# Kernel tuning notes

Measured on AMD Instinct MI355X. Metric: run time of the kernel, lower is better.

Reference implementation:

```python
import jax, jax.numpy as jnp
import numpy as np

HEADS = 8
DIM_HEAD = 64
C = 512              # in_channels == inner_dim = heads*dim_head
WIN = 7              # window size implied by rel_pos table (2*7-1 = 13)
EPS = 1e-5


def setup_inputs() -> dict:
    key = jax.random.key(0)
    ks = jax.random.split(key, 6)
    B = 2048
    inner = HEADS * DIM_HEAD
    x = jax.random.normal(ks[0], (B, C, WIN, WIN), dtype=jnp.float32)
    gamma = jnp.ones((C,), dtype=jnp.float32)
    beta = jnp.zeros((C,), dtype=jnp.float32)
    w_qkv = jax.random.normal(ks[1], (C, 3 * inner), dtype=jnp.float32) / np.sqrt(C)
    rel_table = jax.random.normal(ks[2], (2 * WIN - 1, 2 * WIN - 1, HEADS), dtype=jnp.float32)
    w_out = jax.random.normal(ks[3], (inner, C), dtype=jnp.float32) / np.sqrt(inner)
    b_out = jnp.zeros((C,), dtype=jnp.float32)
    return {"x": x, "gamma": gamma, "beta": beta, "w_qkv": w_qkv,
            "rel_table": rel_table, "w_out": w_out, "b_out": b_out}


def _rel_pos_bias(rel_table, H, W):
    # Swin-style additive bias: bias[h, i, j] = table[hi-hj+H-1, wi-wj+W-1, h]
    hh = jnp.arange(H)
    ww = jnp.arange(W)
    hi = jnp.repeat(hh, W)          # [N] row index of each flattened position
    wi = jnp.tile(ww, H)            # [N] col index
    dh = hi[:, None] - hi[None, :] + (H - 1)   # [N, N]
    dw = wi[:, None] - wi[None, :] + (W - 1)   # [N, N]
    bias = rel_table[dh, dw]        # [N, N, heads]
    return jnp.transpose(bias, (2, 0, 1))      # [heads, N, N]


def reference(x, gamma, beta, w_qkv, rel_table, w_out, b_out):
    B, Cc, H, W = x.shape
    N = H * W
    shortcut = x
    xs = jnp.transpose(x.reshape(B, Cc, N), (0, 2, 1))   # [B, N, C]
    # LayerNorm over channel dim
    mu = jnp.mean(xs, axis=-1, keepdims=True)
    var = jnp.var(xs, axis=-1, keepdims=True)
    xn = (xs - mu) * jax.lax.rsqrt(var + EPS) * gamma + beta
    qkv = xn @ w_qkv                                      # [B, N, 3*inner]
    q, k, v = jnp.split(qkv, 3, axis=-1)
    def heads(t):
        return jnp.transpose(t.reshape(B, N, HEADS, DIM_HEAD), (0, 2, 1, 3))  # [B,h,N,d]
    q, k, v = heads(q), heads(k), heads(v)
    scale = DIM_HEAD ** -0.5
    dots = jnp.einsum('bhnd,bhmd->bhnm', q, k) * scale   # [B,h,N,N]
    dots = dots + _rel_pos_bias(rel_table, H, W)[None]   # add Swin-style bias
    attn = jax.nn.softmax(dots, axis=-1)
    out = jnp.einsum('bhnm,bhmd->bhnd', attn, v)         # [B,h,N,d]
    out = jnp.transpose(out, (0, 2, 1, 3)).reshape(B, N, HEADS * DIM_HEAD)
    out = out @ w_out + b_out                            # [B, N, C]
    out = jnp.transpose(out, (0, 2, 1)).reshape(B, Cc, H, W)
    return out + shortcut
```

## Files before the change

kernel.cpp:

```cpp
#include <hip/hip_runtime.h>

#define BATCH 2048
#define CH 512
#define NTOK 49
#define NHEAD 8
#define DHEAD 64

typedef __attribute__((ext_vector_type(8))) short bf16x8;
typedef __attribute__((ext_vector_type(4))) float f32x4;

__device__ __forceinline__ ushort f2bf(float f) {
  union { float f; unsigned u; } v; v.f = f;
  unsigned r = v.u + 0x7fffu + ((v.u >> 16) & 1u);
  return (ushort)(r >> 16);
}

__device__ __forceinline__ float bf2f(ushort u) {
  union { unsigned u; float f; } v; v.u = ((unsigned)u) << 16;
  return v.f;
}

#define MFMA16(a, b, c) __builtin_amdgcn_mfma_f32_16x16x32_bf16((a), (b), (c), 0, 0, 0)

#define GLOAD_LDS16(gsrc, ldst)                                                  \
  __builtin_amdgcn_global_load_lds((const __attribute__((address_space(1))) void*)(gsrc), \
                                   (__attribute__((address_space(3))) void*)(ldst), 16, 0, 0)

__global__ void prep_kernel(const float* __restrict__ w_qkv, const float* __restrict__ w_out,
                            const float* __restrict__ rel, ushort* __restrict__ wqkvB,
                            ushort* __restrict__ woutF, float* __restrict__ biasP) {
  int tid = blockIdx.x * blockDim.x + threadIdx.x;
  int stride = gridDim.x * blockDim.x;
  for (int i = tid; i < 12 * 16 * 8 * 64 * 8; i += stride) {
    int j = i & 7, lane = (i >> 3) & 63, cbs = (i >> 9) & 7, kk = (i >> 12) & 15, nb = i >> 16;
    int o = nb * 128 + cbs * 16 + (lane & 15);
    int c = kk * 32 + (lane >> 4) * 8 + j;
    wqkvB[i] = f2bf(w_qkv[c * 1536 + o]);
  }
  for (int i = tid; i < 32 * 16 * 64 * 8; i += stride) {
    int j = i & 7, lane = (i >> 3) & 63, ks = (i >> 9) & 15, cb = i >> 13;
    int o = cb * 16 + (lane & 15);
    int c = ks * 32 + (lane >> 4) * 8 + j;
    woutF[i] = f2bf(w_out[c * 512 + o]);
  }
  for (int i = tid; i < NHEAD * 64 * 64; i += stride) {
    int h = i >> 12, n = (i >> 6) & 63, m = i & 63;
    float v = -1e30f;
    if (n < NTOK && m < NTOK) {
      int dh = n / 7 - m / 7 + 6;
      int dw = n % 7 - m % 7 + 6;
      v = rel[(dh * 13 + dw) * 8 + h];
    }
    biasP[i] = v;
  }
}

__global__ __launch_bounds__(256) void ln_kernel(const float* __restrict__ x,
                                                 const float* __restrict__ gamma,
                                                 const float* __restrict__ beta,
                                                 ushort* __restrict__ xnW) {
  int b = blockIdx.x;
  int t = threadIdx.x;
  __shared__ ushort xsb[CH][NTOK];
  __shared__ float muL[64], rsL[64];
  const float4* x4 = (const float4*)(x + (size_t)b * CH * NTOK);
  for (int i4 = t; i4 < CH * NTOK / 4; i4 += 256) {
    float4 v = x4[i4];
    int lf = i4 * 4;
#pragma unroll
    for (int e = 0; e < 4; e++) {
      int idx = lf + e;
      int c = idx / NTOK, n = idx - c * NTOK;
      xsb[c][n] = f2bf(((const float*)&v)[e]);
    }
  }
  __syncthreads();
  int row = t >> 2, sub = t & 3;
  float s = 0.f, s2 = 0.f;
  if (row < NTOK) {
    for (int c = sub; c < CH; c += 4) {
      float v = bf2f(xsb[c][row]);
      s += v;
      s2 += v * v;
    }
  }
  s += __shfl_xor(s, 1);
  s += __shfl_xor(s, 2);
  s2 += __shfl_xor(s2, 1);
  s2 += __shfl_xor(s2, 2);
  if (sub == 0 && row < NTOK) {
    float m = s * (1.f / CH);
    muL[row] = m;
    rsL[row] = rsqrtf(s2 * (1.f / CH) - m * m + 1e-5f);
  }
  __syncthreads();
  ushort* dst = xnW + (size_t)b * NTOK * CH;
  for (int i = t; i < NTOK * 64; i += 256) {
    int n = i >> 6, c0 = (i & 63) * 8;
    float mu = muL[n], rs = rsL[n];
    ushort tmp[8];
#pragma unroll
    for (int j = 0; j < 8; j++) {
      int c = c0 + j;
      tmp[j] = f2bf((bf2f(xsb[c][n]) - mu) * rs * gamma[c] + beta[c]);
    }
    *(uint4*)(dst + (size_t)n * CH + c0) = *(const uint4*)tmp;
  }
}

__global__ __launch_bounds__(256, 4) void qkv_gemm(const ushort* __restrict__ xnW,
                                                   const ushort* __restrict__ wqkvB,
                                                   ushort* __restrict__ qW,
                                                   ushort* __restrict__ kW,
                                                   ushort* __restrict__ vW) {
  int bid = blockIdx.x;
  int f = (bid & 7) * 1176 + (bid >> 3);
  int mb = f / 12, nb = f - mb * 12;
  int r0 = mb * 128;
  int t = threadIdx.x, lane = t & 63, w = t >> 6;
  int wm = w >> 1, wn = w & 1;

  __shared__ __align__(16) ushort lds[8704];

  const int arow = lane & 15, g = lane >> 4;
  int srow0 = w * 16 + (lane >> 2);
  int cL = lane & 3;
  const ushort* wBbase = wqkvB + (size_t)nb * 16 * 4096;
  const ushort* xbase = xnW + (size_t)r0 * CH;

#pragma unroll
  for (int i = 0; i < 2; i++) {
    int row = i * 64 + srow0;
    int cG = cL ^ ((row >> 1) & 3);
    GLOAD_LDS16(xbase + (size_t)row * CH + cG * 8, lds + (i * 64 + w * 16) * 32);
  }
  __syncthreads();

  f32x4 acc[4][4];
#pragma unroll
  for (int mt = 0; mt < 4; mt++)
#pragma unroll
    for (int nt = 0; nt < 4; nt++) acc[mt][nt] = (f32x4){0.f, 0.f, 0.f, 0.f};

  int cur = 0;
  for (int step = 0; step < 16; ++step) {
    const ushort* wp = wBbase + (size_t)step * 4096 + (wn * 4) * 512 + lane * 8;
    bf16x8 bfr[4];
#pragma unroll
    for (int nt = 0; nt < 4; nt++) bfr[nt] = *(const bf16x8*)(wp + nt * 512);
    if (step < 15) {
      int nxt = cur ^ 1, kk = step + 1;
#pragma unroll
      for (int i = 0; i < 2; i++) {
        int row = i * 64 + srow0;
        int cG = cL ^ ((row >> 1) & 3);
        GLOAD_LDS16(xbase + (size_t)row * CH + kk * 32 + cG * 8,
                    lds + nxt * 4096 + (i * 64 + w * 16) * 32);
      }
    }
    const ushort* lA = lds + cur * 4096;
    bf16x8 afr[4];
#pragma unroll
    for (int mt = 0; mt < 4; mt++) {
      int row = wm * 64 + mt * 16 + arow;
      afr[mt] = *(const bf16x8*)&lA[row * 32 + (g ^ ((row >> 1) & 3)) * 8];
    }
#pragma unroll
    for (int mt = 0; mt < 4; mt++)
#pragma unroll
      for (int nt = 0; nt < 4; nt++) acc[mt][nt] = MFMA16(afr[mt], bfr[nt], acc[mt][nt]);
    __syncthreads();
    cur ^= 1;
  }

  ushort(*oL)[136] = (ushort(*)[136])lds;
  int h0 = (nb & 3) * 2;
  int sct = nb >> 2;
#pragma unroll
  for (int hh = 0; hh < 2; hh++) {
    if (wm == hh) {
#pragma unroll
      for (int mt = 0; mt < 4; mt++)
#pragma unroll
        for (int nt = 0; nt < 4; nt++)
#pragma unroll
          for (int r = 0; r < 4; r++) {
            int rn = mt * 16 + 4 * g + r;
            oL[rn][wn * 64 + nt * 16 + arow] = f2bf(acc[mt][nt][r]);
          }
    }
    __syncthreads();
    if (sct < 2) {
      ushort* dst = (sct == 0 ? qW : kW);
      for (int i = t; i < 64 * 16; i += 256) {
        int rn = i >> 4, c8 = i & 15;
        int grow = r0 + hh * 64 + rn;
        int b = grow / 49, n = grow - b * 49;
        int h = h0 + (c8 >> 3);
        *(uint4*)(dst + (size_t)(b * 8 + h) * (NTOK * 64) + n * 64 + (c8 & 7) * 8) =
            *(const uint4*)&oL[rn][c8 * 8];
      }
    } else {
      for (int i = t; i < 64 * 128; i += 256) {
        int rn = i & 63, col = i >> 6;
        int grow = r0 + hh * 64 + rn;
        int b = grow / 49, n = grow - b * 49;
        int h = h0 + (col >> 6), d = col & 63;
        vW[(size_t)(b * 8 + h) * 4096 + d * 64 + n] = oL[rn][col];
      }
    }
    __syncthreads();
  }
}

__global__ __launch_bounds__(512, 4) void attn2(const ushort* __restrict__ qW,
                                                const ushort* __restrict__ kW,
                                                const ushort* __restrict__ vW,
                                                const float* __restrict__ biasP,
                                                ushort* __restrict__ aoW) {
  int b = blockIdx.x;
  int t = threadIdx.x;
  int lane = t & 63;
  int h = t >> 6;

  __shared__ ushort pL[8][64][72];
  ushort(*pl)[72] = pL[h];

  const int c = lane & 15, g = lane >> 4;
  const ushort* qb = qW + (size_t)(b * 8 + h) * NTOK * 64;
  const ushort* kb = kW + (size_t)(b * 8 + h) * NTOK * 64;
  const ushort* vb = vW + (size_t)(b * 8 + h) * 64 * 64;
  const float* bp = biasP + h * 64 * 64;

  f32x4 s[4][4];
#pragma unroll
  for (int mt = 0; mt < 4; mt++)
#pragma unroll
    for (int nt = 0; nt < 4; nt++) s[mt][nt] = (f32x4){0.f, 0.f, 0.f, 0.f};
#pragma unroll
  for (int ks = 0; ks < 2; ks++) {
    bf16x8 kf[4];
#pragma unroll
    for (int nt = 0; nt < 4; nt++)
      kf[nt] = *(const bf16x8*)(kb + (size_t)(nt * 16 + c) * 64 + ks * 32 + g * 8);
#pragma unroll
    for (int mt = 0; mt < 4; mt++) {
      bf16x8 qf = *(const bf16x8*)(qb + (size_t)(mt * 16 + c) * 64 + ks * 32 + g * 8);
#pragma unroll
      for (int nt = 0; nt < 4; nt++) s[mt][nt] = MFMA16(qf, kf[nt], s[mt][nt]);
    }
  }
#pragma unroll
  for (int mt = 0; mt < 4; mt++)
#pragma unroll
    for (int nt = 0; nt < 4; nt++)
#pragma unroll
      for (int r = 0; r < 4; r++) {
        int n = mt * 16 + 4 * g + r;
        int m = nt * 16 + c;
        s[mt][nt][r] = s[mt][nt][r] * 0.125f + bp[n * 64 + m];
      }

#pragma unroll
  for (int mt = 0; mt < 4; mt++)
#pragma unroll
    for (int r = 0; r < 4; r++) {
      float mx = fmaxf(fmaxf(s[mt][0][r], s[mt][1][r]), fmaxf(s[mt][2][r], s[mt][3][r]));
      mx = fmaxf(mx, __shfl_xor(mx, 1));
      mx = fmaxf(mx, __shfl_xor(mx, 2));
      mx = fmaxf(mx, __shfl_xor(mx, 4));
      mx = fmaxf(mx, __shfl_xor(mx, 8));
      float p0 = __expf(s[mt][0][r] - mx);
      float p1 = __expf(s[mt][1][r] - mx);
      float p2 = __expf(s[mt][2][r] - mx);
      float p3 = __expf(s[mt][3][r] - mx);
      float sum = p0 + p1 + p2 + p3;
      sum += __shfl_xor(sum, 1);
      sum += __shfl_xor(sum, 2);
      sum += __shfl_xor(sum, 4);
      sum += __shfl_xor(sum, 8);
      float rinv = 1.f / sum;
      int n = mt * 16 + 4 * g + r;
      pl[n][0 * 16 + c] = f2bf(p0 * rinv);
      pl[n][1 * 16 + c] = f2bf(p1 * rinv);
      pl[n][2 * 16 + c] = f2bf(p2 * rinv);
      pl[n][3 * 16 + c] = f2bf(p3 * rinv);
    }

  f32x4 o[4][4];
#pragma unroll
  for (int mt = 0; mt < 4; mt++)
#pragma unroll
    for (int nt = 0; nt < 4; nt++) o[mt][nt] = (f32x4){0.f, 0.f, 0.f, 0.f};
#pragma unroll
  for (int ks = 0; ks < 2; ks++) {
    bf16x8 vf[4];
#pragma unroll
    for (int nt = 0; nt < 4; nt++)
      vf[nt] = *(const bf16x8*)(vb + (size_t)(nt * 16 + c) * 64 + ks * 32 + g * 8);
#pragma unroll
    for (int mt = 0; mt < 4; mt++) {
      bf16x8 pf = *(const bf16x8*)&pl[mt * 16 + c][ks * 32 + g * 8];
#pragma unroll
      for (int nt = 0; nt < 4; nt++) o[mt][nt] = MFMA16(pf, vf[nt], o[mt][nt]);
    }
  }

#pragma unroll
  for (int mt = 0; mt < 4; mt++)
#pragma unroll
    for (int nt = 0; nt < 4; nt++)
#pragma unroll
      for (int r = 0; r < 4; r++) {
        int n = mt * 16 + 4 * g + r;
        pl[n][nt * 16 + c] = f2bf(o[mt][nt][r]);
      }
  ushort* ao = aoW + (size_t)b * NTOK * CH + h * 64;
  for (int i = lane; i < NTOK * 8; i += 64) {
    int row = i >> 3, c8 = i & 7;
    *(uint4*)(ao + (size_t)row * CH + c8 * 8) = *(const uint4*)&pl[row][c8 * 8];
  }
}

__global__ __launch_bounds__(256, 4) void proj_kernel(const ushort* __restrict__ aoW,
                                                      const ushort* __restrict__ woutF,
                                                      const float* __restrict__ b_out,
                                                      const float* __restrict__ x,
                                                      float* __restrict__ out) {
  int bid = blockIdx.x;
  int f = (bid & 7) * 512 + (bid >> 3);
  int mb = f >> 2, nbp = f & 3;
  int b0 = mb * 2;
  int t = threadIdx.x, lane = t & 63, w = t >> 6;
  int wm = w >> 1, wn = w & 1;

  __shared__ __align__(16) char ldsraw[33792];
  ushort* lds = (ushort*)ldsraw;
  float(*oL)[132] = (float(*)[132])ldsraw;

  for (int i = t; i < 2 * 30 * 32; i += 256) {
    int buf = i >= 960;
    int r2 = i - buf * 960;
    int rr = r2 >> 5;
    int row = (rr < 15) ? (49 + rr) : (98 + rr);
    lds[buf * 4096 + row * 32 + (i & 31)] = 0;
  }

  const int arow = lane & 15, g = lane >> 4;
  int srow0 = w * 16 + (lane >> 2);
  int cL = lane & 3;

  {
#pragma unroll
    for (int i = 0; i < 2; i++) {
      int row = i * 64 + srow0;
      int n = row & 63, bb = b0 + (row >> 6);
      int cG = cL ^ ((row >> 1) & 3);
      if (n < NTOK)
        GLOAD_LDS16(aoW + ((size_t)bb * NTOK + n) * CH + cG * 8, lds + (i * 64 + w * 16) * 32);
    }
  }
  __syncthreads();

  f32x4 acc[4][4];
#pragma unroll
  for (int mt = 0; mt < 4; mt++)
#pragma unroll
    for (int nt = 0; nt < 4; nt++) acc[mt][nt] = (f32x4){0.f, 0.f, 0.f, 0.f};

  int cur = 0;
  for (int step = 0; step < 16; ++step) {
    const ushort* wp = woutF + ((size_t)(nbp * 8 + wn * 4) * 16 + step) * 512 + lane * 8;
    bf16x8 bfr[4];
#pragma unroll
    for (int nt = 0; nt < 4; nt++) bfr[nt] = *(const bf16x8*)(wp + (size_t)nt * 16 * 512);
    if (step < 15) {
      int nxt = cur ^ 1, kk = step + 1;
#pragma unroll
      for (int i = 0; i < 2; i++) {
        int row = i * 64 + srow0;
        int n = row & 63, bb = b0 + (row >> 6);
        int cG = cL ^ ((row >> 1) & 3);
        if (n < NTOK)
          GLOAD_LDS16(aoW + ((size_t)bb * NTOK + n) * CH + kk * 32 + cG * 8,
                      lds + nxt * 4096 + (i * 64 + w * 16) * 32);
      }
    }
    const ushort* lA = lds + cur * 4096;
    bf16x8 afr[4];
#pragma unroll
    for (int mt = 0; mt < 4; mt++) {
      int row = wm * 64 + mt * 16 + arow;
      afr[mt] = *(const bf16x8*)&lA[row * 32 + (g ^ ((row >> 1) & 3)) * 8];
    }
#pragma unroll
    for (int mt = 0; mt < 4; mt++)
#pragma unroll
      for (int nt = 0; nt < 4; nt++) acc[mt][nt] = MFMA16(afr[mt], bfr[nt], acc[mt][nt]);
    __syncthreads();
    cur ^= 1;
  }

  const float* bo = b_out + nbp * 128;
#pragma unroll
  for (int hh = 0; hh < 2; hh++) {
    if (wm == hh) {
#pragma unroll
      for (int mt = 0; mt < 4; mt++)
#pragma unroll
        for (int nt = 0; nt < 4; nt++)
#pragma unroll
          for (int r = 0; r < 4; r++) {
            int rn = mt * 16 + 4 * g + r;
            if (rn < NTOK) oL[rn][wn * 64 + nt * 16 + arow] = acc[mt][nt][r];
          }
    }
    __syncthreads();
    int b = b0 + hh;
    const float4* x4 = (const float4*)(x + ((size_t)b * CH + nbp * 128) * NTOK);
    float4* o4 = (float4*)(out + ((size_t)b * CH + nbp * 128) * NTOK);
    for (int i = t; i < 1568; i += 256) {
      float4 xv = x4[i];
      float4 ov;
      int lf = i * 4;
#pragma unroll
      for (int e = 0; e < 4; e++) {
        int cl = (lf + e) / NTOK, n = (lf + e) - cl * NTOK;
        ((float*)&ov)[e] = oL[n][cl] + bo[cl] + ((const float*)&xv)[e];
      }
      o4[i] = ov;
    }
    __syncthreads();
  }
}

extern "C" void kernel_launch(void* const* d_in, const int* in_sizes, int n_in,
                              void* d_out, int out_size, void* d_ws, size_t ws_size,
                              hipStream_t stream) {
  const float* x = (const float*)d_in[0];
  const float* gamma = (const float*)d_in[1];
  const float* beta = (const float*)d_in[2];
  const float* w_qkv = (const float*)d_in[3];
  const float* rel = (const float*)d_in[4];
  const float* w_out = (const float*)d_in[5];
  const float* b_out = (const float*)d_in[6];
  float* out = (float*)d_out;

  char* ws = (char*)d_ws;
  size_t off = 0;
  ushort* wqkvB = (ushort*)(ws + off); off += (size_t)12 * 16 * 4096 * 2;
  ushort* woutF = (ushort*)(ws + off); off += (size_t)512 * 512 * 2;
  float* biasP = (float*)(ws + off);   off += (size_t)NHEAD * 64 * 64 * 4;
  ushort* qW = (ushort*)(ws + off);    off += ((size_t)BATCH * 8 * NTOK * 64 + 1024) * 2;
  ushort* kW = (ushort*)(ws + off);    off += ((size_t)BATCH * 8 * NTOK * 64 + 1024) * 2;
  ushort* vW = (ushort*)(ws + off);    off += (size_t)BATCH * 8 * 64 * 64 * 2;
  ushort* xnW = (ushort*)(ws + off);   off += (size_t)BATCH * NTOK * CH * 2;
  ushort* aoW = xnW;
  (void)ws_size;

  prep_kernel<<<1024, 256, 0, stream>>>(w_qkv, w_out, rel, wqkvB, woutF, biasP);
  ln_kernel<<<BATCH, 256, 0, stream>>>(x, gamma, beta, xnW);
  qkv_gemm<<<784 * 12, 256, 0, stream>>>(xnW, wqkvB, qW, kW, vW);
  attn2<<<BATCH, 512, 0, stream>>>(qW, kW, vW, biasP, aoW);
  proj_kernel<<<BATCH / 2 * 4, 256, 0, stream>>>(aoW, woutF, b_out, x, out);
}
```

Baseline: 617.9 us.

## Deepen QKV GEMM k-tile, fold q scale, split attention to one-wave blocks

The QKV GEMM now stages 64-wide K tiles (8 stages instead of 16) with an XOR swizzle over 8 chunks, which halves barrier count but doubles LDS use. The 1/sqrt(d) scale is folded into the Q store. The relative-position bias is repacked into MFMA fragment order so attention reads it as float4 per lane. Attention is launched as one 64-thread block per (batch, head) with s_setprio around the MFMA sections. The smaller LDS footprint per block is meant to raise occupancy and scheduling flexibility, at the cost of many more tiny blocks.

```diff
diff --git a/kernel.cpp b/kernel.cpp
--- a/kernel.cpp
+++ b/kernel.cpp
@@ -28,7 +28,7 @@
 
 __global__ void prep_kernel(const float* __restrict__ w_qkv, const float* __restrict__ w_out,
                             const float* __restrict__ rel, ushort* __restrict__ wqkvB,
-                            ushort* __restrict__ woutF, float* __restrict__ biasP) {
+                            ushort* __restrict__ woutF, float* __restrict__ biasF) {
   int tid = blockIdx.x * blockDim.x + threadIdx.x;
   int stride = gridDim.x * blockDim.x;
   for (int i = tid; i < 12 * 16 * 8 * 64 * 8; i += stride) {
@@ -43,15 +43,23 @@
     int c = ks * 32 + (lane >> 4) * 8 + j;
     woutF[i] = f2bf(w_out[c * 512 + o]);
   }
-  for (int i = tid; i < NHEAD * 64 * 64; i += stride) {
-    int h = i >> 12, n = (i >> 6) & 63, m = i & 63;
-    float v = -1e30f;
-    if (n < NTOK && m < NTOK) {
-      int dh = n / 7 - m / 7 + 6;
-      int dw = n % 7 - m % 7 + 6;
-      v = rel[(dh * 13 + dw) * 8 + h];
-    }
-    biasP[i] = v;
+  for (int i = tid; i < NHEAD * 4 * 4 * 64; i += stride) {
+    int lane = i & 63, nt = (i >> 6) & 3, mt = (i >> 8) & 3, h = i >> 10;
+    int cc = lane & 15, g = lane >> 4;
+    float4 v;
+#pragma unroll
+    for (int r = 0; r < 4; r++) {
+      int n = mt * 16 + 4 * g + r;
+      int m = nt * 16 + cc;
+      float bv = -1e30f;
+      if (n < NTOK && m < NTOK) {
+        int dh = n / 7 - m / 7 + 6;
+        int dw = n % 7 - m % 7 + 6;
+        bv = rel[(dh * 13 + dw) * 8 + h];
+      }
+      ((float*)&v)[r] = bv;
+    }
+    ((float4*)biasF)[i] = v;
   }
 }
 
@@ -120,19 +128,20 @@
   int t = threadIdx.x, lane = t & 63, w = t >> 6;
   int wm = w >> 1, wn = w & 1;
 
-  __shared__ __align__(16) ushort lds[8704];
+  __shared__ __align__(16) ushort lds[16384];
 
   const int arow = lane & 15, g = lane >> 4;
-  int srow0 = w * 16 + (lane >> 2);
-  int cL = lane & 3;
   const ushort* wBbase = wqkvB + (size_t)nb * 16 * 4096;
   const ushort* xbase = xnW + (size_t)r0 * CH;
 
-#pragma unroll
-  for (int i = 0; i < 2; i++) {
-    int row = i * 64 + srow0;
-    int cG = cL ^ ((row >> 1) & 3);
-    GLOAD_LDS16(xbase + (size_t)row * CH + cG * 8, lds + (i * 64 + w * 16) * 32);
+  int drow = t >> 3;
+  int slot = t & 7;
+  int gchunk = slot ^ (drow & 7);
+
+#pragma unroll
+  for (int i = 0; i < 4; i++) {
+    int row = drow + i * 32;
+    GLOAD_LDS16(xbase + (size_t)row * CH + gchunk * 8, lds + i * 2048 + t * 8);
   }
   __syncthreads();
 
@@ -143,32 +152,34 @@
     for (int nt = 0; nt < 4; nt++) acc[mt][nt] = (f32x4){0.f, 0.f, 0.f, 0.f};
 
   int cur = 0;
-  for (int step = 0; step < 16; ++step) {
-    const ushort* wp = wBbase + (size_t)step * 4096 + (wn * 4) * 512 + lane * 8;
-    bf16x8 bfr[4];
-#pragma unroll
-    for (int nt = 0; nt < 4; nt++) bfr[nt] = *(const bf16x8*)(wp + nt * 512);
-    if (step < 15) {
-      int nxt = cur ^ 1, kk = step + 1;
-#pragma unroll
-      for (int i = 0; i < 2; i++) {
-        int row = i * 64 + srow0;
-        int cG = cL ^ ((row >> 1) & 3);
-        GLOAD_LDS16(xbase + (size_t)row * CH + kk * 32 + cG * 8,
-                    lds + nxt * 4096 + (i * 64 + w * 16) * 32);
-      }
-    }
-    const ushort* lA = lds + cur * 4096;
-    bf16x8 afr[4];
-#pragma unroll
-    for (int mt = 0; mt < 4; mt++) {
-      int row = wm * 64 + mt * 16 + arow;
-      afr[mt] = *(const bf16x8*)&lA[row * 32 + (g ^ ((row >> 1) & 3)) * 8];
-    }
-#pragma unroll
-    for (int mt = 0; mt < 4; mt++)
-#pragma unroll
-      for (int nt = 0; nt < 4; nt++) acc[mt][nt] = MFMA16(afr[mt], bfr[nt], acc[mt][nt]);
+  for (int stage = 0; stage < 8; ++stage) {
+    if (stage < 7) {
+      int nxt = cur ^ 1, kk = stage + 1;
+#pragma unroll
+      for (int i = 0; i < 4; i++) {
+        GLOAD_LDS16(xbase + (size_t)(drow + i * 32) * CH + kk * 64 + gchunk * 8,
+                    lds + nxt * 8192 + i * 2048 + t * 8);
+      }
+    }
+    const ushort* lA = lds + cur * 8192;
+#pragma unroll
+    for (int ks = 0; ks < 2; ks++) {
+      int kk2 = stage * 2 + ks;
+      const ushort* wp = wBbase + (size_t)kk2 * 4096 + (wn * 4) * 512 + lane * 8;
+      bf16x8 bfr[4];
+#pragma unroll
+      for (int nt = 0; nt < 4; nt++) bfr[nt] = *(const bf16x8*)(wp + nt * 512);
+      bf16x8 afr[4];
+#pragma unroll
+      for (int mt = 0; mt < 4; mt++) {
+        int row = wm * 64 + mt * 16 + arow;
+        afr[mt] = *(const bf16x8*)&lA[row * 64 + ((ks * 4 + g) ^ (arow & 7)) * 8];
+      }
+#pragma unroll
+      for (int mt = 0; mt < 4; mt++)
+#pragma unroll
+        for (int nt = 0; nt < 4; nt++) acc[mt][nt] = MFMA16(afr[mt], bfr[nt], acc[mt][nt]);
+    }
     __syncthreads();
     cur ^= 1;
   }
@@ -176,6 +187,7 @@
   ushort(*oL)[136] = (ushort(*)[136])lds;
   int h0 = (nb & 3) * 2;
   int sct = nb >> 2;
+  float sc = (sct == 0) ? 0.125f : 1.0f;
 #pragma unroll
   for (int hh = 0; hh < 2; hh++) {
     if (wm == hh) {
@@ -186,7 +198,7 @@
 #pragma unroll
           for (int r = 0; r < 4; r++) {
             int rn = mt * 16 + 4 * g + r;
-            oL[rn][wn * 64 + nt * 16 + arow] = f2bf(acc[mt][nt][r]);
+            oL[rn][wn * 64 + nt * 16 + arow] = f2bf(acc[mt][nt][r] * sc);
           }
     }
     __syncthreads();
@@ -213,30 +225,29 @@
   }
 }
 
-__global__ __launch_bounds__(512, 4) void attn2(const ushort* __restrict__ qW,
+__global__ __launch_bounds__(64, 4) void attn1w(const ushort* __restrict__ qW,
                                                 const ushort* __restrict__ kW,
                                                 const ushort* __restrict__ vW,
-                                                const float* __restrict__ biasP,
+                                                const float* __restrict__ biasF,
                                                 ushort* __restrict__ aoW) {
-  int b = blockIdx.x;
-  int t = threadIdx.x;
-  int lane = t & 63;
-  int h = t >> 6;
-
-  __shared__ ushort pL[8][64][72];
-  ushort(*pl)[72] = pL[h];
+  int bid = blockIdx.x;
+  int b = bid >> 3, h = bid & 7;
+  int lane = threadIdx.x;
+
+  __shared__ ushort pl[64][72];
 
   const int c = lane & 15, g = lane >> 4;
   const ushort* qb = qW + (size_t)(b * 8 + h) * NTOK * 64;
   const ushort* kb = kW + (size_t)(b * 8 + h) * NTOK * 64;
   const ushort* vb = vW + (size_t)(b * 8 + h) * 64 * 64;
-  const float* bp = biasP + h * 64 * 64;
+  const float4* bf = (const float4*)biasF + (size_t)h * 16 * 64;
 
   f32x4 s[4][4];
 #pragma unroll
   for (int mt = 0; mt < 4; mt++)
 #pragma unroll
     for (int nt = 0; nt < 4; nt++) s[mt][nt] = (f32x4){0.f, 0.f, 0.f, 0.f};
+  __builtin_amdgcn_s_setprio(1);
 #pragma unroll
   for (int ks = 0; ks < 2; ks++) {
     bf16x8 kf[4];
@@ -250,16 +261,16 @@
       for (int nt = 0; nt < 4; nt++) s[mt][nt] = MFMA16(qf, kf[nt], s[mt][nt]);
     }
   }
-#pragma unroll
-  for (int mt = 0; mt < 4; mt++)
-#pragma unroll
-    for (int nt = 0; nt < 4; nt++)
-#pragma unroll
-      for (int r = 0; r < 4; r++) {
-        int n = mt * 16 + 4 * g + r;
-        int m = nt * 16 + c;
-        s[mt][nt][r] = s[mt][nt][r] * 0.125f + bp[n * 64 + m];
-      }
+  __builtin_amdgcn_s_setprio(0);
+
+#pragma unroll
+  for (int mt = 0; mt < 4; mt++)
+#pragma unroll
+    for (int nt = 0; nt < 4; nt++) {
+      float4 bb = bf[(mt * 4 + nt) * 64 + lane];
+#pragma unroll
+      for (int r = 0; r < 4; r++) s[mt][nt][r] += ((const float*)&bb)[r];
+    }
 
 #pragma unroll
   for (int mt = 0; mt < 4; mt++)
@@ -292,6 +303,7 @@
   for (int mt = 0; mt < 4; mt++)
 #pragma unroll
     for (int nt = 0; nt < 4; nt++) o[mt][nt] = (f32x4){0.f, 0.f, 0.f, 0.f};
+  __builtin_amdgcn_s_setprio(1);
 #pragma unroll
   for (int ks = 0; ks < 2; ks++) {
     bf16x8 vf[4];
@@ -305,6 +317,7 @@
       for (int nt = 0; nt < 4; nt++) o[mt][nt] = MFMA16(pf, vf[nt], o[mt][nt]);
     }
   }
+  __builtin_amdgcn_s_setprio(0);
 
 #pragma unroll
   for (int mt = 0; mt < 4; mt++)
@@ -450,7 +463,7 @@
   size_t off = 0;
   ushort* wqkvB = (ushort*)(ws + off); off += (size_t)12 * 16 * 4096 * 2;
   ushort* woutF = (ushort*)(ws + off); off += (size_t)512 * 512 * 2;
-  float* biasP = (float*)(ws + off);   off += (size_t)NHEAD * 64 * 64 * 4;
+  float* biasF = (float*)(ws + off);   off += (size_t)NHEAD * 16 * 64 * 4 * 4;
   ushort* qW = (ushort*)(ws + off);    off += ((size_t)BATCH * 8 * NTOK * 64 + 1024) * 2;
   ushort* kW = (ushort*)(ws + off);    off += ((size_t)BATCH * 8 * NTOK * 64 + 1024) * 2;
   ushort* vW = (ushort*)(ws + off);    off += (size_t)BATCH * 8 * 64 * 64 * 2;
@@ -458,9 +471,9 @@
   ushort* aoW = xnW;
   (void)ws_size;
 
-  prep_kernel<<<1024, 256, 0, stream>>>(w_qkv, w_out, rel, wqkvB, woutF, biasP);
+  prep_kernel<<<1024, 256, 0, stream>>>(w_qkv, w_out, rel, wqkvB, woutF, biasF);
   ln_kernel<<<BATCH, 256, 0, stream>>>(x, gamma, beta, xnW);
   qkv_gemm<<<784 * 12, 256, 0, stream>>>(xnW, wqkvB, qW, kW, vW);
-  attn2<<<BATCH, 512, 0, stream>>>(qW, kW, vW, biasP, aoW);
+  attn1w<<<BATCH * NHEAD, 64, 0, stream>>>(qW, kW, vW, biasF, aoW);
   proj_kernel<<<BATCH / 2 * 4, 256, 0, stream>>>(aoW, woutF, b_out, x, out);
 }
```

New measurement: 627.1 us. Within noise of the previous version (+1.5%).
